# Kernel tuning notes

Measured on AMD Instinct MI355X. Metric: run time of the kernel, lower is better.

The kernel has to match this reference:

```python
import jax, jax.numpy as jnp
import numpy as np

T, D, E, K = 8192, 4096, 64, 8


def setup_inputs() -> dict:
    key = jax.random.key(0)
    k1, k2, k3, k4 = jax.random.split(key, 4)
    x = jax.random.normal(k1, (T, D), dtype=jnp.float32)
    # nn.Linear stores weight as [out_features, in_features]
    Wg = jax.random.normal(k2, (E, D), dtype=jnp.float32) * (1.0 / np.sqrt(D))
    Wc = jax.random.normal(k3, (E, D), dtype=jnp.float32) * (1.0 / np.sqrt(D))
    extra_scale = jnp.zeros((E,), dtype=jnp.float32)  # init zeros as in module
    extra_bias = jax.random.normal(k4, (E,), dtype=jnp.float32) * 0.01
    return {"x": x, "Wg": Wg, "Wc": Wc, "extra_scale": extra_scale,
            "extra_bias": extra_bias, "topk": K}


def reference(x, Wg, Wc, extra_scale, extra_bias, topk):
    # scores = |classifier(x) * silu(gate(x))|, softmax in fp32
    gate = jnp.einsum('td,ed->te', x, Wg)        # [T, E]
    cls = jnp.einsum('td,ed->te', x, Wc)         # [T, E]
    scores = jnp.abs(cls * jax.nn.silu(gate))
    scores = jax.nn.softmax(scores.astype(jnp.float32), axis=-1)
    biased = scores + extra_bias[None, :]        # load-balance bias, used only for selection
    _, indices = jax.lax.top_k(biased, topk)     # [T, K]
    original = 1.0 + scores * extra_scale[None, :]
    weights = jnp.take_along_axis(original, indices, axis=1)  # [T, K]
    return weights.astype(x.dtype), indices
```

## Files before the change

kernel.cpp:

```cpp
#include <hip/hip_runtime.h>
#include <math.h>


#define T_DIM 8192
#define D_DIM 4096
#define E_DIM 64
#define N2    128
#define MB    128
#define BK    32
#define LDA   132
#define KTOP  8

__global__ __launch_bounds__(256, 2)
void router_gemm(const float* __restrict__ x,
                 const float* __restrict__ Wg,
                 const float* __restrict__ Wc,
                 float* __restrict__ P,
                 int sliceK)
{
    __shared__ float sx[BK][LDA];
    __shared__ float sw[BK][LDA];

    const int tid = threadIdx.x;
    const int mb  = blockIdx.x;
    const int ks  = blockIdx.y;

    const int r2 = tid >> 1;
    const int kq = tid & 1;

    const int k0 = ks * sliceK;

    const float4* xp = (const float4*)(x + (size_t)(mb * MB + r2) * D_DIM + k0 + kq * 16);
    const float*  wrow = (r2 < E_DIM) ? (Wg + (size_t)r2 * D_DIM)
                                      : (Wc + (size_t)(r2 - E_DIM) * D_DIM);
    const float4* wp = (const float4*)(wrow + k0 + kq * 16);

    float4 rx[4], rw[4];
    #pragma unroll
    for (int q = 0; q < 4; ++q) { rx[q] = xp[q]; rw[q] = wp[q]; }

    float acc[8][8];
    #pragma unroll
    for (int i = 0; i < 8; ++i)
        #pragma unroll
        for (int j = 0; j < 8; ++j) acc[i][j] = 0.f;

    const int tm8 = (tid & 15) * 8;
    const int tn8 = (tid >> 4) * 8;
    const int NS  = sliceK / BK;

    for (int s = 0; s < NS; ++s) {
        #pragma unroll
        for (int q = 0; q < 4; ++q) {
            const int k = kq * 16 + q * 4;
            sx[k+0][r2] = rx[q].x; sx[k+1][r2] = rx[q].y;
            sx[k+2][r2] = rx[q].z; sx[k+3][r2] = rx[q].w;
            sw[k+0][r2] = rw[q].x; sw[k+1][r2] = rw[q].y;
            sw[k+2][r2] = rw[q].z; sw[k+3][r2] = rw[q].w;
        }
        __syncthreads();

        if (s + 1 < NS) {
            xp += 8; wp += 8;
            #pragma unroll
            for (int q = 0; q < 4; ++q) { rx[q] = xp[q]; rw[q] = wp[q]; }
        }

        #pragma unroll
        for (int kk = 0; kk < BK; ++kk) {
            const float4 a0 = *(const float4*)&sx[kk][tm8];
            const float4 a1 = *(const float4*)&sx[kk][tm8 + 4];
            const float4 b0 = *(const float4*)&sw[kk][tn8];
            const float4 b1 = *(const float4*)&sw[kk][tn8 + 4];
            const float a[8] = {a0.x,a0.y,a0.z,a0.w,a1.x,a1.y,a1.z,a1.w};
            const float b[8] = {b0.x,b0.y,b0.z,b0.w,b1.x,b1.y,b1.z,b1.w};
            #pragma unroll
            for (int i = 0; i < 8; ++i)
                #pragma unroll
                for (int j = 0; j < 8; ++j)
                    acc[i][j] = fmaf(a[i], b[j], acc[i][j]);
        }
        __syncthreads();
    }

    float* Pr = P + ((size_t)ks * T_DIM + (size_t)mb * MB + tm8) * N2 + tn8;
    #pragma unroll
    for (int i = 0; i < 8; ++i) {
        const float4 s0 = make_float4(acc[i][0], acc[i][1], acc[i][2], acc[i][3]);
        const float4 s1 = make_float4(acc[i][4], acc[i][5], acc[i][6], acc[i][7]);
        *(float4*)&Pr[(size_t)i * N2]     = s0;
        *(float4*)&Pr[(size_t)i * N2 + 4] = s1;
    }
}

__global__ __launch_bounds__(256)
void router_topk(const float* __restrict__ P,
                 const float* __restrict__ scale,
                 const float* __restrict__ bias,
                 float* __restrict__ out,
                 int ksplit)
{
    const int lane = threadIdx.x & 63;
    const int wid  = threadIdx.x >> 6;
    const int row  = blockIdx.x * 4 + wid;

    float g = 0.f, c = 0.f;
    for (int ks = 0; ks < ksplit; ++ks) {
        const float* p = P + ((size_t)ks * T_DIM + row) * N2;
        g += p[lane];
        c += p[E_DIM + lane];
    }
    const float sg = g / (1.f + expf(-g));
    const float v  = fabsf(c * sg);

    float m = v;
    #pragma unroll
    for (int off = 32; off >= 1; off >>= 1) m = fmaxf(m, __shfl_xor(m, off));
    const float e = expf(v - m);
    float Z = e;
    #pragma unroll
    for (int off = 32; off >= 1; off >>= 1) Z += __shfl_xor(Z, off);
    const float s = e / Z;

    const float sc  = scale[lane];
    float cur = s + bias[lane];

    float myw = 0.f; int myi = 0;
    #pragma unroll
    for (int j = 0; j < KTOP; ++j) {
        float bv = cur; int bi = lane;
        #pragma unroll
        for (int off = 32; off >= 1; off >>= 1) {
            const float ov = __shfl_xor(bv, off);
            const int   oi = __shfl_xor(bi, off);
            if (ov > bv || (ov == bv && oi < bi)) { bv = ov; bi = oi; }
        }
        const float s_bi  = __shfl(s,  bi);
        const float sc_bi = __shfl(sc, bi);
        const float w = 1.f + s_bi * sc_bi;
        if (lane == j)  { myw = w; myi = bi; }
        if (lane == bi) cur = -INFINITY;
    }

    if (lane < KTOP) {
        out[(size_t)row * KTOP + lane] = myw;
        out[(size_t)T_DIM * KTOP + (size_t)row * KTOP + lane] = (float)myi;
    }
}

extern "C" void kernel_launch(void* const* d_in, const int* in_sizes, int n_in,
                              void* d_out, int out_size, void* d_ws, size_t ws_size,
                              hipStream_t stream)
{
    const float* x  = (const float*)d_in[0];
    const float* Wg = (const float*)d_in[1];
    const float* Wc = (const float*)d_in[2];
    const float* sc = (const float*)d_in[3];
    const float* bs = (const float*)d_in[4];
    float* out = (float*)d_out;
    float* P   = (float*)d_ws;

    int ksplit = 8;
    const size_t per = (size_t)T_DIM * N2 * sizeof(float);
    while (ksplit > 1 && (size_t)ksplit * per > ws_size) ksplit >>= 1;
    const int sliceK = D_DIM / ksplit;

    dim3 g1(T_DIM / MB, ksplit);
    router_gemm<<<g1, 256, 0, stream>>>(x, Wg, Wc, P, sliceK);
    router_topk<<<T_DIM / 4, 256, 0, stream>>>(P, sc, bs, out, ksplit);
}
```

Baseline: 268.4 us.

## Swizzle LDS layout, template split-K, raise occupancy and split to 16

Pads and swizzles the shared-memory tile indices to cut LDS bank conflicts on the transposed stores and the float4 reads. Split-K becomes a template parameter so loop counts are compile-time, and the reduce kernel loads all partials at once before summing. The launch-bounds occupancy hint goes from 2 to 4 blocks per SIMD, and the default split rises from 8 to 16 when workspace allows. The higher occupancy hint may force register spills given the 64-accumulator tile, and a split of 16 doubles the partial-sum traffic the top-k kernel must read.

```diff
diff --git a/kernel.cpp b/kernel.cpp
--- a/kernel.cpp
+++ b/kernel.cpp
@@ -8,16 +8,21 @@
 #define N2    128
 #define MB    128
 #define BK    32
-#define LDA   132
+#define LDA   140
 #define KTOP  8
 
-__global__ __launch_bounds__(256, 2)
+__device__ __forceinline__ int SW(int m) { return m + ((m >> 5) << 2); }
+
+template<int KS>
+__global__ __launch_bounds__(256, 4)
 void router_gemm(const float* __restrict__ x,
                  const float* __restrict__ Wg,
                  const float* __restrict__ Wc,
-                 float* __restrict__ P,
-                 int sliceK)
+                 float* __restrict__ P)
 {
+    constexpr int SLICEK = D_DIM / KS;
+    constexpr int NS     = SLICEK / BK;
+
     __shared__ float sx[BK][LDA];
     __shared__ float sw[BK][LDA];
 
@@ -28,7 +33,7 @@
     const int r2 = tid >> 1;
     const int kq = tid & 1;
 
-    const int k0 = ks * sliceK;
+    const int k0 = ks * SLICEK;
 
     const float4* xp = (const float4*)(x + (size_t)(mb * MB + r2) * D_DIM + k0 + kq * 16);
     const float*  wrow = (r2 < E_DIM) ? (Wg + (size_t)r2 * D_DIM)
@@ -47,16 +52,18 @@
 
     const int tm8 = (tid & 15) * 8;
     const int tn8 = (tid >> 4) * 8;
-    const int NS  = sliceK / BK;
+    const int smx = SW(tm8);
+    const int snx = SW(tn8);
+    const int swr = SW(r2);
 
     for (int s = 0; s < NS; ++s) {
         #pragma unroll
         for (int q = 0; q < 4; ++q) {
             const int k = kq * 16 + q * 4;
-            sx[k+0][r2] = rx[q].x; sx[k+1][r2] = rx[q].y;
-            sx[k+2][r2] = rx[q].z; sx[k+3][r2] = rx[q].w;
-            sw[k+0][r2] = rw[q].x; sw[k+1][r2] = rw[q].y;
-            sw[k+2][r2] = rw[q].z; sw[k+3][r2] = rw[q].w;
+            sx[k+0][swr] = rx[q].x; sx[k+1][swr] = rx[q].y;
+            sx[k+2][swr] = rx[q].z; sx[k+3][swr] = rx[q].w;
+            sw[k+0][swr] = rw[q].x; sw[k+1][swr] = rw[q].y;
+            sw[k+2][swr] = rw[q].z; sw[k+3][swr] = rw[q].w;
         }
         __syncthreads();
 
@@ -68,10 +75,10 @@
 
         #pragma unroll
         for (int kk = 0; kk < BK; ++kk) {
-            const float4 a0 = *(const float4*)&sx[kk][tm8];
-            const float4 a1 = *(const float4*)&sx[kk][tm8 + 4];
-            const float4 b0 = *(const float4*)&sw[kk][tn8];
-            const float4 b1 = *(const float4*)&sw[kk][tn8 + 4];
+            const float4 a0 = *(const float4*)&sx[kk][smx];
+            const float4 a1 = *(const float4*)&sx[kk][smx + 4];
+            const float4 b0 = *(const float4*)&sw[kk][snx];
+            const float4 b1 = *(const float4*)&sw[kk][snx + 4];
             const float a[8] = {a0.x,a0.y,a0.z,a0.w,a1.x,a1.y,a1.z,a1.w};
             const float b[8] = {b0.x,b0.y,b0.z,b0.w,b1.x,b1.y,b1.z,b1.w};
             #pragma unroll
@@ -93,23 +100,28 @@
     }
 }
 
+template<int KS>
 __global__ __launch_bounds__(256)
 void router_topk(const float* __restrict__ P,
                  const float* __restrict__ scale,
                  const float* __restrict__ bias,
-                 float* __restrict__ out,
-                 int ksplit)
+                 float* __restrict__ out)
 {
     const int lane = threadIdx.x & 63;
     const int wid  = threadIdx.x >> 6;
     const int row  = blockIdx.x * 4 + wid;
 
+    float gv[KS], cv[KS];
+    #pragma unroll
+    for (int ks = 0; ks < KS; ++ks) {
+        const float* p = P + ((size_t)ks * T_DIM + row) * N2;
+        gv[ks] = p[lane];
+        cv[ks] = p[E_DIM + lane];
+    }
     float g = 0.f, c = 0.f;
-    for (int ks = 0; ks < ksplit; ++ks) {
-        const float* p = P + ((size_t)ks * T_DIM + row) * N2;
-        g += p[lane];
-        c += p[E_DIM + lane];
-    }
+    #pragma unroll
+    for (int ks = 0; ks < KS; ++ks) { g += gv[ks]; c += cv[ks]; }
+
     const float sg = g / (1.f + expf(-g));
     const float v  = fabsf(c * sg);
 
@@ -148,6 +160,16 @@
     }
 }
 
+template<int KS>
+static void launch_all(const float* x, const float* Wg, const float* Wc,
+                       const float* sc, const float* bs,
+                       float* out, float* P, hipStream_t stream)
+{
+    dim3 g1(T_DIM / MB, KS);
+    router_gemm<KS><<<g1, 256, 0, stream>>>(x, Wg, Wc, P);
+    router_topk<KS><<<T_DIM / 4, 256, 0, stream>>>(P, sc, bs, out);
+}
+
 extern "C" void kernel_launch(void* const* d_in, const int* in_sizes, int n_in,
                               void* d_out, int out_size, void* d_ws, size_t ws_size,
                               hipStream_t stream)
@@ -160,12 +182,15 @@
     float* out = (float*)d_out;
     float* P   = (float*)d_ws;
 
-    int ksplit = 8;
     const size_t per = (size_t)T_DIM * N2 * sizeof(float);
+    int ksplit = 16;
     while (ksplit > 1 && (size_t)ksplit * per > ws_size) ksplit >>= 1;
-    const int sliceK = D_DIM / ksplit;
 
-    dim3 g1(T_DIM / MB, ksplit);
-    router_gemm<<<g1, 256, 0, stream>>>(x, Wg, Wc, P, sliceK);
-    router_topk<<<T_DIM / 4, 256, 0, stream>>>(P, sc, bs, out, ksplit);
+    switch (ksplit) {
+        case 16: launch_all<16>(x, Wg, Wc, sc, bs, out, P, stream); break;
+        case 8:  launch_all<8>(x, Wg, Wc, sc, bs, out, P, stream); break;
+        case 4:  launch_all<4>(x, Wg, Wc, sc, bs, out, P, stream); break;
+        case 2:  launch_all<2>(x, Wg, Wc, sc, bs, out, P, stream); break;
+        default: launch_all<1>(x, Wg, Wc, sc, bs, out, P, stream); break;
+    }
 }
```

Result: slower. 717.4 us (+167.2%).
